# Optimization experiments

Measured on AMD Instinct MI355X. Metric: run time of the kernel, lower is better.

Reference implementation:

```python
import jax, jax.numpy as jnp
import numpy as np

N_NODES = 25000
N_EDGES = 400000
F_IN = 6
H = 128
NUM_CLASSES = 21
NUM_GAUSS = 16
Z_DIM = 2 * H + NUM_GAUSS  # 272


def setup_inputs() -> dict:
    key = jax.random.key(0)
    ks = jax.random.split(key, 16)
    inp = {
        "x": jax.random.normal(ks[0], (N_NODES, F_IN), dtype=jnp.float32),
        "edge_attr": jax.random.uniform(ks[1], (N_EDGES,), dtype=jnp.float32) * 8.0,
        "node_w": jax.random.normal(ks[2], (F_IN, H), dtype=jnp.float32) * 0.1,
        "node_b": jnp.zeros((H,), jnp.float32),
        "f1_w": jax.random.normal(ks[3], (Z_DIM, H), dtype=jnp.float32) * 0.05,
        "f1_b": jnp.zeros((H,), jnp.float32),
        "s1_w": jax.random.normal(ks[4], (Z_DIM, H), dtype=jnp.float32) * 0.05,
        "s1_b": jnp.zeros((H,), jnp.float32),
        "bn1_g": jnp.ones((H,), jnp.float32),
        "bn1_b": jnp.zeros((H,), jnp.float32),
        "f2_w": jax.random.normal(ks[5], (Z_DIM, H), dtype=jnp.float32) * 0.05,
        "f2_b": jnp.zeros((H,), jnp.float32),
        "s2_w": jax.random.normal(ks[6], (Z_DIM, H), dtype=jnp.float32) * 0.05,
        "s2_b": jnp.zeros((H,), jnp.float32),
        "bn2_g": jnp.ones((H,), jnp.float32),
        "bn2_b": jnp.zeros((H,), jnp.float32),
        "fc_w": jax.random.normal(ks[7], (H, NUM_CLASSES), dtype=jnp.float32) * 0.05,
        "fc_b": jnp.zeros((NUM_CLASSES,), jnp.float32),
        "edge_index": jax.random.randint(ks[8], (2, N_EDGES), 0, N_NODES, dtype=jnp.int64),
    }
    return inp


def gaussian_smearing(dist):
    # start=0, stop=8, num_gaussians=16
    offset = jnp.linspace(0.0, 8.0, NUM_GAUSS)
    coeff = -0.5 / (8.0 / (NUM_GAUSS - 1)) ** 2
    d = dist[:, None] - offset[None, :]  # [E, 16]
    return jnp.exp(coeff * d * d)


def cgconv(x, src, dst, e, fw, fb, sw, sb, gamma, beta):
    # PyG CGConv: z = cat([x_i, x_j, e]); msg = sigmoid(lin_f(z)) * softplus(lin_s(z))
    # aggr='add' into target i, then BatchNorm1d, then residual +x
    z = jnp.concatenate([x[dst], x[src], e], axis=-1)  # [E, 2H+16]
    msg = jax.nn.sigmoid(z @ fw + fb) * jax.nn.softplus(z @ sw + sb)  # [E, H]
    agg = jax.ops.segment_sum(msg, dst, num_segments=x.shape[0])  # [N, H]
    mu = jnp.mean(agg, axis=0)
    var = jnp.var(agg, axis=0)
    agg = (agg - mu) * jax.lax.rsqrt(var + 1e-5) * gamma + beta
    return agg + x


def reference(x, edge_attr, node_w, node_b, f1_w, f1_b, s1_w, s1_b, bn1_g, bn1_b,
              f2_w, f2_b, s2_w, s2_b, bn2_g, bn2_b, fc_w, fc_b, edge_index):
    src, dst = edge_index[0], edge_index[1]
    e = gaussian_smearing(edge_attr)  # [E, 16]
    h = x @ node_w + node_b  # [N, H]
    h = cgconv(h, src, dst, e, f1_w, f1_b, s1_w, s1_b, bn1_g, bn1_b)
    h = jax.nn.relu(h)
    # dropout p=0.1 is identity in eval mode
    h = cgconv(h, src, dst, e, f2_w, f2_b, s2_w, s2_b, bn2_g, bn2_b)
    h = jax.nn.relu(h)
    return h @ fc_w + fc_b  # [N, 21]
```

## Files before the change

kernel.cpp:

```cpp
#include <hip/hip_runtime.h>
#include <hip/hip_bf16.h>
#include <math.h>

#define NN 25000
#define NE 400000
#define HH 128
#define NH (NN*HH)
#define NBINS 2048

#define GS_STEP  (8.0f/15.0f)
#define GS_COEFF (-1.7578125f)
#define LOG2E    1.442695041f
#define LN2      0.6931471806f
#define BINSC    ((float)NBINS / 8.0f)

typedef float f32x2 __attribute__((ext_vector_type(2)));
typedef float f32x4 __attribute__((ext_vector_type(4)));
typedef short bf16x8 __attribute__((ext_vector_type(8)));

__device__ __forceinline__ f32x2 bf2_unpack(unsigned int u) {
  union { unsigned int i; float f; } lo, hi;
  lo.i = u << 16;
  hi.i = u & 0xffff0000u;
  f32x2 r; r.x = lo.f; r.y = hi.f;
  return r;
}

__device__ __forceinline__ unsigned short bf16_of(float f) {
  return __hip_bfloat16_raw(__float2bfloat16(f)).x;
}

__global__ __launch_bounds__(256) void k_prep(
    const float* __restrict__ f1w, const float* __restrict__ s1w,
    const float* __restrict__ f1b, const float* __restrict__ s1b,
    const float* __restrict__ f2w, const float* __restrict__ s2w,
    const float* __restrict__ f2b, const float* __restrict__ s2b,
    unsigned short* __restrict__ Wf1, float* __restrict__ bv1,
    unsigned short* __restrict__ L1,
    unsigned short* __restrict__ Wf2, float* __restrict__ bv2,
    unsigned short* __restrict__ L2, float* __restrict__ statsall,
    int* __restrict__ deg) {
  const int layer = blockIdx.y;
  const float* fw = layer ? f2w : f1w;
  const float* sw = layer ? s2w : s1w;
  const float* fb = layer ? f2b : f1b;
  const float* sb = layer ? s2b : s1b;
  unsigned short* Wf = layer ? Wf2 : Wf1;
  float* biasv = layer ? bv2 : bv1;
  unsigned short* LUT = layer ? L2 : L1;
  const int bx = blockIdx.x;
  const int tid = threadIdx.x;
  if (bx < 256) {
    if (bx == 0) statsall[layer * 256 + tid] = 0.f;
    if (layer == 0 && bx < 98) {
      const int i = bx * 256 + tid;
      if (i < NN) deg[i] = 0;
    }
    const int t = bx * 256 + tid;
    if (t < 512) biasv[t] = (t < 256) ? ((t & 1) ? sb[t >> 1] : fb[t >> 1]) : 0.f;
    const int j = t & 7;
    const int lane = (t >> 3) & 63;
    const int kt = (t >> 9) & 3;
    const int nt = t >> 11;
    const int k = 32 * kt + 8 * (lane >> 4) + j;
    const int c = 16 * nt + (lane & 15);
    const int cc = c & 255;
    const int row = ((c >= 256) ? 128 : 0) + k;
    const float* m = (cc & 1) ? sw : fw;
    Wf[t] = bf16_of(m[row * HH + (cc >> 1)]);
  } else {
    const int bin = (bx - 256) * 2 + (tid >> 7);
    if (bin > NBINS) return;
    const int j = tid & 127;
    const float* fw3 = fw + 256 * HH;
    const float* sw3 = sw + 256 * HH;
    const float d = (float)bin * (8.0f / (float)NBINS);
    f32x2 acc = 0.f;
#pragma unroll
    for (int k = 0; k < 16; ++k) {
      float tt = d - (float)k * GS_STEP;
      float ee = __expf(GS_COEFF * tt * tt);
      f32x2 w;
      w.x = fw3[k * HH + j];
      w.y = sw3[k * HH + j];
      acc = __builtin_elementwise_fma((f32x2)(ee), w, acc);
    }
    *(unsigned int*)&LUT[bin * 256 + 2 * j] =
        (unsigned int)bf16_of(acc.x) | ((unsigned int)bf16_of(acc.y) << 16);
  }
}

__device__ __forceinline__ void gemm_core(
    const unsigned short* As, const unsigned short* __restrict__ Wfrag,
    const float* __restrict__ biasv, int n0, int bn0,
    unsigned short* __restrict__ PDh, unsigned short* __restrict__ PSh,
    int tid) {
  const int w = tid >> 6;
  const int lane = tid & 63;
  const int mt0 = 2 * w;
  f32x4 acc[2][8];
#pragma unroll
  for (int mi = 0; mi < 2; ++mi)
#pragma unroll
    for (int nt = 0; nt < 8; ++nt) acc[mi][nt] = (f32x4)0.f;
  const int ntg0 = bn0 >> 4;
#pragma unroll
  for (int kt = 0; kt < 4; ++kt) {
    const bf16x8 a0 = *(const bf16x8*)&As[((mt0 * 4 + kt) * 64 + lane) * 8];
    const bf16x8 a1 = *(const bf16x8*)&As[(((mt0 + 1) * 4 + kt) * 64 + lane) * 8];
#pragma unroll
    for (int nt = 0; nt < 8; ++nt) {
      const bf16x8 b =
          *(const bf16x8*)&Wfrag[(((ntg0 + nt) * 4 + kt) * 64 + lane) * 8];
      acc[0][nt] = __builtin_amdgcn_mfma_f32_16x16x32_bf16(a0, b, acc[0][nt], 0, 0, 0);
      acc[1][nt] = __builtin_amdgcn_mfma_f32_16x16x32_bf16(a1, b, acc[1][nt], 0, 0, 0);
    }
  }
  const int colloc = lane & 15;
  const int rbase = (lane >> 4) * 4;
  const bool isPD = (bn0 < 256);
#pragma unroll
  for (int mi = 0; mi < 2; ++mi) {
#pragma unroll
    for (int nt = 0; nt < 8; ++nt) {
      const int c = bn0 + nt * 16 + colloc;
      const float bias = biasv[c];
#pragma unroll
      for (int r = 0; r < 4; ++r) {
        const int n = n0 + (mt0 + mi) * 16 + rbase + r;
        if (n < NN) {
          const float vv = acc[mi][nt][r] + bias;
          if (isPD) PDh[n * 256 + c] = bf16_of(vv);
          else PSh[n * 256 + (c - 256)] = bf16_of(vv);
        }
      }
    }
  }
}

__global__ __launch_bounds__(256) void k_gemm1(
    const float* __restrict__ x, const float* __restrict__ nw,
    const float* __restrict__ nb, const unsigned short* __restrict__ Wfrag,
    const float* __restrict__ biasv, float* __restrict__ h0,
    unsigned short* __restrict__ PDh, unsigned short* __restrict__ PSh,
    float* __restrict__ zb) {
  __shared__ unsigned short As[128 * 128];
  __shared__ float wn[6 * 128 + 128];
  const int tid = threadIdx.x;
  const int n0 = blockIdx.x * 128;
  const int bn0 = blockIdx.y * 128;
  const bool wr_h0 = (blockIdx.y == 0);
  for (int i = tid; i < 6 * 128 + 128; i += 256)
    wn[i] = (i < 6 * 128) ? nw[i] : nb[i - 6 * 128];
  if (blockIdx.y == 1) {
    const float4 z = {0.f, 0.f, 0.f, 0.f};
    for (int i = tid; i < 128 * 32; i += 256) {
      const int n = n0 + (i >> 5);
      if (n < NN) *(float4*)&zb[n * HH + (i & 31) * 4] = z;
    }
  }
  __syncthreads();
  {
    const int tn = tid >> 2;
    const int cj = tid & 3;
#pragma unroll
    for (int ii = 0; ii < 2; ++ii) {
      const int n = tn + 64 * ii;
      const int gn = n0 + n;
      float xr[6];
      if (gn < NN) {
#pragma unroll
        for (int q = 0; q < 6; ++q) xr[q] = x[gn * 6 + q];
      }
#pragma unroll
      for (int i = 0; i < 4; ++i) {
        const int c = cj + 4 * i;
        bf16x8 bv = (bf16x8)0;
        if (gn < NN) {
          float4 r0, r1;
#pragma unroll
          for (int j = 0; j < 8; ++j) {
            const int k = c * 8 + j;
            float acc = wn[6 * 128 + k];
#pragma unroll
            for (int q = 0; q < 6; ++q) acc = fmaf(xr[q], wn[q * 128 + k], acc);
            if (j < 4) (&r0.x)[j] = acc; else (&r1.x)[j - 4] = acc;
            bv[j] = (short)bf16_of(acc);
          }
          if (wr_h0) {
            *(float4*)&h0[gn * HH + c * 8] = r0;
            *(float4*)&h0[gn * HH + c * 8 + 4] = r1;
          }
        }
        const int slot = ((n >> 4) * 4 + (c >> 2)) * 64 + (n & 15) + 16 * (c & 3);
        *(bf16x8*)&As[slot * 8] = bv;
      }
    }
  }
  __syncthreads();
  gemm_core(As, Wfrag, biasv, n0, bn0, PDh, PSh, tid);
}

__global__ __launch_bounds__(256) void k_gemm_mfma(
    const float* __restrict__ h, const unsigned short* __restrict__ Wfrag,
    const float* __restrict__ biasv,
    unsigned short* __restrict__ PDh, unsigned short* __restrict__ PSh) {
  __shared__ unsigned short As[128 * 128];
  const int tid = threadIdx.x;
  const int n0 = blockIdx.x * 128;
  const int bn0 = blockIdx.y * 128;
  {
    const int tn = tid >> 2;
    const int cj = tid & 3;
#pragma unroll
    for (int ii = 0; ii < 2; ++ii) {
      const int n = tn + 64 * ii;
      const int gn = n0 + n;
#pragma unroll
      for (int i = 0; i < 4; ++i) {
        const int c = cj + 4 * i;
        bf16x8 bv;
        if (gn < NN) {
          const float4 p0 = *(const float4*)&h[gn * HH + c * 8];
          const float4 p1 = *(const float4*)&h[gn * HH + c * 8 + 4];
          bv[0] = (short)bf16_of(p0.x); bv[1] = (short)bf16_of(p0.y);
          bv[2] = (short)bf16_of(p0.z); bv[3] = (short)bf16_of(p0.w);
          bv[4] = (short)bf16_of(p1.x); bv[5] = (short)bf16_of(p1.y);
          bv[6] = (short)bf16_of(p1.z); bv[7] = (short)bf16_of(p1.w);
        } else {
          bv = (bf16x8)0;
        }
        const int slot = ((n >> 4) * 4 + (c >> 2)) * 64 + (n & 15) + 16 * (c & 3);
        *(bf16x8*)&As[slot * 8] = bv;
      }
    }
  }
  __syncthreads();
  gemm_core(As, Wfrag, biasv, n0, bn0, PDh, PSh, tid);
}

__global__ __launch_bounds__(256) void k_hist(
    const int* __restrict__ ei, int* __restrict__ deg, int* __restrict__ rank) {
  int e = blockIdx.x * 256 + threadIdx.x;
  if (e < NE) rank[e] = atomicAdd(&deg[ei[NE + e]], 1);
}

__global__ __launch_bounds__(1024) void k_scan(
    const int* __restrict__ deg, int* __restrict__ rowptr) {
  __shared__ int part[1024];
  const int tid = threadIdx.x;
  const int CH = (NN + 1023) / 1024;
  const int base = tid * CH;
  int s = 0;
  for (int i = 0; i < CH; ++i) {
    int n = base + i;
    if (n < NN) s += deg[n];
  }
  part[tid] = s;
  __syncthreads();
  for (int off = 1; off < 1024; off <<= 1) {
    int t = (tid >= off) ? part[tid - off] : 0;
    __syncthreads();
    part[tid] += t;
    __syncthreads();
  }
  int run = part[tid] - s;
  for (int i = 0; i < CH; ++i) {
    int n = base + i;
    if (n < NN) {
      rowptr[n] = run;
      run += deg[n];
    }
  }
}

__global__ __launch_bounds__(256) void k_scatter(
    const int* __restrict__ ei, const float* __restrict__ eattr,
    const int* __restrict__ rowptr, const int* __restrict__ rank,
    int2* __restrict__ emeta) {
  int e = blockIdx.x * 256 + threadIdx.x;
  if (e >= NE) return;
  const int dst = ei[NE + e];
  const int src = ei[e];
  const int bin = (int)(eattr[e] * BINSC + 0.5f);
  const int pos = rowptr[dst] + rank[e];
  emeta[pos] = make_int2(src | (dst << 16), bin << 8);
}

__global__ __launch_bounds__(256) void k_edge_sorted(
    const int2* __restrict__ emeta, const unsigned short* __restrict__ LUTh,
    const unsigned short* __restrict__ PDh, const unsigned short* __restrict__ PSh,
    float* __restrict__ agg) {
  const int tid = threadIdx.x;
  const int lane = tid & 63;
  const int w = __builtin_amdgcn_readfirstlane(tid >> 6);
  const int bid = blockIdx.x;
  const int xcd = bid & 7;
  const int idx = bid >> 3;
  const int sb = ((xcd < 5) ? xcd * 391 : 5 * 391 + (xcd - 5) * 390) + idx;
  const int e0 = sb * 128 + w * 32;
  const int u4 = 4 * lane;
  float m0 = 0.f, m1 = 0.f;
  int cur = -1;
  f32x2 a0 = 0.f, a1 = 0.f;
  uint2 b[4], v[4];
#pragma unroll
  for (int p = 0; p < 4; ++p) {
    const int2 md = emeta[e0 + p];
    b[p] = *(const uint2*)&PSh[((md.x & 0xffff) << 8) + u4];
    v[p] = *(const uint2*)&LUTh[md.y + u4];
  }
#pragma unroll
  for (int it = 0; it < 32; ++it) {
    const int sl = it & 3;
    const int dst = (int)((unsigned)emeta[e0 + it].x >> 16);
    if (dst != cur) {
      const uint2 ad = *(const uint2*)&PDh[(dst << 8) + u4];
      a0 = bf2_unpack(ad.x);
      a1 = bf2_unpack(ad.y);
      cur = dst;
    }
    const f32x2 bb0 = bf2_unpack(b[sl].x);
    const f32x2 bb1 = bf2_unpack(b[sl].y);
    const f32x2 w0 = bf2_unpack(v[sl].x);
    const f32x2 w1 = bf2_unpack(v[sl].y);
    if (it < 28) {
      const int2 mn = emeta[e0 + it + 4];
      b[sl] = *(const uint2*)&PSh[((mn.x & 0xffff) << 8) + u4];
      v[sl] = *(const uint2*)&LUTh[mn.y + u4];
    }
    const f32x2 fs0 = (a0 + bb0) + w0;
    const f32x2 fs1 = (a1 + bb1) + w1;
    const float ef0 = __builtin_amdgcn_exp2f(-fs0.x * LOG2E);
    const float ef1 = __builtin_amdgcn_exp2f(-fs1.x * LOG2E);
    const float et0 = __builtin_amdgcn_exp2f(-fabsf(fs0.y) * LOG2E);
    const float et1 = __builtin_amdgcn_exp2f(-fabsf(fs1.y) * LOG2E);
    const float sig0 = __builtin_amdgcn_rcpf(1.f + ef0);
    const float sig1 = __builtin_amdgcn_rcpf(1.f + ef1);
    const float sp0 = fmaxf(fs0.y, 0.f) + LN2 * __builtin_amdgcn_logf(1.f + et0);
    const float sp1 = fmaxf(fs1.y, 0.f) + LN2 * __builtin_amdgcn_logf(1.f + et1);
    m0 = fmaf(sig0, sp0, m0);
    m1 = fmaf(sig1, sp1, m1);
    bool fl = true;
    if (it < 31) fl = ((int)((unsigned)emeta[e0 + it + 1].x >> 16) != dst);
    if (fl) {
      atomicAdd(&agg[dst * HH + 2 * lane], m0);
      atomicAdd(&agg[dst * HH + 2 * lane + 1], m1);
      m0 = 0.f;
      m1 = 0.f;
    }
  }
}

__global__ __launch_bounds__(256) void k_stats(
    const float* __restrict__ agg, float* __restrict__ stats) {
  const int c = threadIdx.x & 127;
  const int slice = (blockIdx.x * 256 + threadIdx.x) >> 7;
  const int nslices = (gridDim.x * 256) >> 7;
  float s = 0.f, s2 = 0.f;
  for (int n = slice; n < NN; n += nslices) {
    float v = agg[n * HH + c];
    s += v;
    s2 = fmaf(v, v, s2);
  }
  atomicAdd(&stats[c], s);
  atomicAdd(&stats[HH + c], s2);
}

__global__ __launch_bounds__(256) void k_bn(
    const float* __restrict__ agg, float* __restrict__ hold,
    const float* __restrict__ stats, const float* __restrict__ g,
    const float* __restrict__ b, float* __restrict__ hnew) {
  int t = blockIdx.x * 256 + threadIdx.x;
  if (t >= NH) return;
  const int c = t & 127;
  const float inv_n = 1.f / (float)NN;
  const float mu = stats[c] * inv_n;
  const float var = stats[HH + c] * inv_n - mu * mu;
  const float rs = rsqrtf(var + 1e-5f);
  const float v = (agg[t] - mu) * rs * g[c] + b[c] + hold[t];
  hnew[t] = fmaxf(v, 0.f);
  hold[t] = 0.f;
}

__global__ __launch_bounds__(256) void k_fc(
    const float* __restrict__ agg, const float* __restrict__ hold,
    const float* __restrict__ stats, const float* __restrict__ g,
    const float* __restrict__ bb, const float* __restrict__ w,
    const float* __restrict__ b, float* __restrict__ out) {
  __shared__ float hs[8][128];
  __shared__ float scale[128], shift[128];
  const int tid = threadIdx.x;
  const int n0 = blockIdx.x * 8;
  if (tid < 128) {
    const float inv_n = 1.f / (float)NN;
    const float mu = stats[tid] * inv_n;
    const float var = stats[128 + tid] * inv_n - mu * mu;
    const float sc = rsqrtf(var + 1e-5f) * g[tid];
    scale[tid] = sc;
    shift[tid] = bb[tid] - mu * sc;
  }
  __syncthreads();
  {
    const int nl = tid >> 5;
    const int k0 = (tid & 31) * 4;
    const int gn = n0 + nl;
    if (gn < NN) {
      const float4 av = *(const float4*)&agg[gn * HH + k0];
      const float4 ov = *(const float4*)&hold[gn * HH + k0];
#pragma unroll
      for (int jj = 0; jj < 4; ++jj) {
        const int k = k0 + jj;
        const float a = (&av.x)[jj], o = (&ov.x)[jj];
        hs[nl][k] = fmaxf(fmaf(a, scale[k], shift[k]) + o, 0.f);
      }
    }
  }
  __syncthreads();
  const int ln = tid >> 5;
  const int m = tid & 31;
  const int n = n0 + ln;
  if (n >= NN || m >= 21) return;
  float acc = b[m];
#pragma unroll 4
  for (int k = 0; k < HH; ++k) acc = fmaf(hs[ln][k], w[k * 21 + m], acc);
  out[n * 21 + m] = acc;
}

extern "C" void kernel_launch(void* const* d_in, const int* in_sizes, int n_in,
                              void* d_out, int out_size, void* d_ws, size_t ws_size,
                              hipStream_t stream) {
  const float* x      = (const float*)d_in[0];
  const float* eattr  = (const float*)d_in[1];
  const float* node_w = (const float*)d_in[2];
  const float* node_b = (const float*)d_in[3];
  const float* f1w    = (const float*)d_in[4];
  const float* f1b    = (const float*)d_in[5];
  const float* s1w    = (const float*)d_in[6];
  const float* s1b    = (const float*)d_in[7];
  const float* bn1g   = (const float*)d_in[8];
  const float* bn1b   = (const float*)d_in[9];
  const float* f2w    = (const float*)d_in[10];
  const float* f2b    = (const float*)d_in[11];
  const float* s2w    = (const float*)d_in[12];
  const float* s2b    = (const float*)d_in[13];
  const float* bn2g   = (const float*)d_in[14];
  const float* bn2b   = (const float*)d_in[15];
  const float* fcw    = (const float*)d_in[16];
  const float* fcb    = (const float*)d_in[17];
  const int*   ei     = (const int*)d_in[18];
  float* out = (float*)d_out;

  float* ws   = (float*)d_ws;
  float* bufA = ws;
  float* bufB = ws + NH;
  unsigned short* PDh = (unsigned short*)(ws + 2 * (size_t)NH);
  unsigned short* PSh = (unsigned short*)(ws + 3 * (size_t)NH);
  float* stats1 = ws + 4 * (size_t)NH;
  float* stats2 = stats1 + 256;
  int*   deg    = (int*)(stats2 + 256);
  int*   rowptr = deg + NN;
  int*   rank   = rowptr + NN;
  int2*  emeta  = (int2*)(rank + NE);
  unsigned short* Wf1 = (unsigned short*)(emeta + NE);
  float* bv1    = (float*)(Wf1 + 65536);
  unsigned short* Wf2 = (unsigned short*)(bv1 + 512);
  float* bv2    = (float*)(Wf2 + 65536);
  unsigned short* lut1 = (unsigned short*)(bv2 + 512);
  unsigned short* lut2 = lut1 + (size_t)(NBINS + 1) * 256;

  const int g_edge  = NE / 128;
  const int g_bn    = (NH + 255) / 256;
  const int g_e256  = (NE + 255) / 256;
  const dim3 g_gemm((NN + 127) / 128, 4);
  const dim3 g_prep(256 + (NBINS + 2 + 1) / 2, 2);

  k_prep<<<g_prep, 256, 0, stream>>>(f1w, s1w, f1b, s1b, f2w, s2w, f2b, s2b,
                                     Wf1, bv1, lut1, Wf2, bv2, lut2,
                                     stats1, deg);

  k_hist<<<g_e256, 256, 0, stream>>>(ei, deg, rank);
  k_scan<<<1, 1024, 0, stream>>>(deg, rowptr);
  k_scatter<<<g_e256, 256, 0, stream>>>(ei, eattr, rowptr, rank, emeta);

  k_gemm1<<<g_gemm, 256, 0, stream>>>(x, node_w, node_b, Wf1, bv1, bufA,
                                      PDh, PSh, bufB);
  k_edge_sorted<<<g_edge, 256, 0, stream>>>(emeta, lut1, PDh, PSh, bufB);
  k_stats<<<256, 256, 0, stream>>>(bufB, stats1);
  k_bn<<<g_bn, 256, 0, stream>>>(bufB, bufA, stats1, bn1g, bn1b, bufB);

  k_gemm_mfma<<<g_gemm, 256, 0, stream>>>(bufB, Wf2, bv2, PDh, PSh);
  k_edge_sorted<<<g_edge, 256, 0, stream>>>(emeta, lut2, PDh, PSh, bufA);
  k_stats<<<256, 256, 0, stream>>>(bufA, stats2);

  k_fc<<<(NN + 7) / 8, 256, 0, stream>>>(bufA, bufB, stats2, bn2g, bn2b,
                                         fcw, fcb, out);
}
```

Before: 303.2 us.

## Fuse histogram into prep kernel, prefetch dst rows, vectorize stats

Three changes. The degree-histogram kernel is folded into the prep launch as a third grid slice, and deg is cleared with a memset. The edge kernel now prefetches the next distinct destination's PDh row a few edges ahead, so the gather latency at segment boundaries is hidden. The BN stats kernel reads float4 per thread on half as many blocks. Fusing the histogram saves one launch, but it adds a memset, and the prep grid now includes idle blocks.

```diff
diff --git a/kernel.cpp b/kernel.cpp
--- a/kernel.cpp
+++ b/kernel.cpp
@@ -39,7 +39,16 @@
     unsigned short* __restrict__ L1,
     unsigned short* __restrict__ Wf2, float* __restrict__ bv2,
     unsigned short* __restrict__ L2, float* __restrict__ statsall,
-    int* __restrict__ deg) {
+    int* __restrict__ deg, const int* __restrict__ ei,
+    int* __restrict__ rank) {
+  const int bx = blockIdx.x;
+  const int tid = threadIdx.x;
+  if (blockIdx.y == 2) {
+    int e = bx * 256 + tid;
+    if (e < NE) rank[e] = atomicAdd(&deg[ei[NE + e]], 1);
+    return;
+  }
+  if (bx >= 1281) return;
   const int layer = blockIdx.y;
   const float* fw = layer ? f2w : f1w;
   const float* sw = layer ? s2w : s1w;
@@ -48,14 +57,8 @@
   unsigned short* Wf = layer ? Wf2 : Wf1;
   float* biasv = layer ? bv2 : bv1;
   unsigned short* LUT = layer ? L2 : L1;
-  const int bx = blockIdx.x;
-  const int tid = threadIdx.x;
   if (bx < 256) {
     if (bx == 0) statsall[layer * 256 + tid] = 0.f;
-    if (layer == 0 && bx < 98) {
-      const int i = bx * 256 + tid;
-      if (i < NN) deg[i] = 0;
-    }
     const int t = bx * 256 + tid;
     if (t < 512) biasv[t] = (t < 256) ? ((t & 1) ? sb[t >> 1] : fb[t >> 1]) : 0.f;
     const int j = t & 7;
@@ -239,12 +242,6 @@
   gemm_core(As, Wfrag, biasv, n0, bn0, PDh, PSh, tid);
 }
 
-__global__ __launch_bounds__(256) void k_hist(
-    const int* __restrict__ ei, int* __restrict__ deg, int* __restrict__ rank) {
-  int e = blockIdx.x * 256 + threadIdx.x;
-  if (e < NE) rank[e] = atomicAdd(&deg[ei[NE + e]], 1);
-}
-
 __global__ __launch_bounds__(1024) void k_scan(
     const int* __restrict__ deg, int* __restrict__ rowptr) {
   __shared__ int part[1024];
@@ -304,6 +301,8 @@
   int cur = -1;
   f32x2 a0 = 0.f, a1 = 0.f;
   uint2 b[4], v[4];
+  int pend_dst = (int)((unsigned)emeta[e0].x >> 16);
+  uint2 pend = *(const uint2*)&PDh[(pend_dst << 8) + u4];
 #pragma unroll
   for (int p = 0; p < 4; ++p) {
     const int2 md = emeta[e0 + p];
@@ -315,7 +314,9 @@
     const int sl = it & 3;
     const int dst = (int)((unsigned)emeta[e0 + it].x >> 16);
     if (dst != cur) {
-      const uint2 ad = *(const uint2*)&PDh[(dst << 8) + u4];
+      uint2 ad;
+      if (dst == pend_dst) ad = pend;
+      else ad = *(const uint2*)&PDh[(dst << 8) + u4];
       a0 = bf2_unpack(ad.x);
       a1 = bf2_unpack(ad.y);
       cur = dst;
@@ -328,6 +329,12 @@
       const int2 mn = emeta[e0 + it + 4];
       b[sl] = *(const uint2*)&PSh[((mn.x & 0xffff) << 8) + u4];
       v[sl] = *(const uint2*)&LUTh[mn.y + u4];
+      const int d4 = (int)((unsigned)mn.x >> 16);
+      const int d3 = (int)((unsigned)emeta[e0 + it + 3].x >> 16);
+      if (d4 != d3) {
+        pend = *(const uint2*)&PDh[(d4 << 8) + u4];
+        pend_dst = d4;
+      }
     }
     const f32x2 fs0 = (a0 + bb0) + w0;
     const f32x2 fs1 = (a1 + bb1) + w1;
@@ -354,17 +361,23 @@
 
 __global__ __launch_bounds__(256) void k_stats(
     const float* __restrict__ agg, float* __restrict__ stats) {
-  const int c = threadIdx.x & 127;
-  const int slice = (blockIdx.x * 256 + threadIdx.x) >> 7;
-  const int nslices = (gridDim.x * 256) >> 7;
-  float s = 0.f, s2 = 0.f;
+  const int c4 = (threadIdx.x & 31) * 4;
+  const int slice = blockIdx.x * 8 + (threadIdx.x >> 5);
+  const int nslices = gridDim.x * 8;
+  f32x4 s = (f32x4)0.f, s2 = (f32x4)0.f;
   for (int n = slice; n < NN; n += nslices) {
-    float v = agg[n * HH + c];
-    s += v;
-    s2 = fmaf(v, v, s2);
-  }
-  atomicAdd(&stats[c], s);
-  atomicAdd(&stats[HH + c], s2);
+    const float4 vv = *(const float4*)&agg[n * HH + c4];
+    s.x += vv.x; s.y += vv.y; s.z += vv.z; s.w += vv.w;
+    s2.x = fmaf(vv.x, vv.x, s2.x);
+    s2.y = fmaf(vv.y, vv.y, s2.y);
+    s2.z = fmaf(vv.z, vv.z, s2.z);
+    s2.w = fmaf(vv.w, vv.w, s2.w);
+  }
+#pragma unroll
+  for (int j = 0; j < 4; ++j) {
+    atomicAdd(&stats[c4 + j], s[j]);
+    atomicAdd(&stats[HH + c4 + j], s2[j]);
+  }
 }
 
 __global__ __launch_bounds__(256) void k_bn(
@@ -473,25 +486,26 @@
   const int g_bn    = (NH + 255) / 256;
   const int g_e256  = (NE + 255) / 256;
   const dim3 g_gemm((NN + 127) / 128, 4);
-  const dim3 g_prep(256 + (NBINS + 2 + 1) / 2, 2);
+  const dim3 g_prep(1563, 3);
+
+  hipMemsetAsync(deg, 0, NN * 4, stream);
 
   k_prep<<<g_prep, 256, 0, stream>>>(f1w, s1w, f1b, s1b, f2w, s2w, f2b, s2b,
                                      Wf1, bv1, lut1, Wf2, bv2, lut2,
-                                     stats1, deg);
-
-  k_hist<<<g_e256, 256, 0, stream>>>(ei, deg, rank);
+                                     stats1, deg, ei, rank);
+
   k_scan<<<1, 1024, 0, stream>>>(deg, rowptr);
   k_scatter<<<g_e256, 256, 0, stream>>>(ei, eattr, rowptr, rank, emeta);
 
   k_gemm1<<<g_gemm, 256, 0, stream>>>(x, node_w, node_b, Wf1, bv1, bufA,
                                       PDh, PSh, bufB);
   k_edge_sorted<<<g_edge, 256, 0, stream>>>(emeta, lut1, PDh, PSh, bufB);
-  k_stats<<<256, 256, 0, stream>>>(bufB, stats1);
+  k_stats<<<128, 256, 0, stream>>>(bufB, stats1);
   k_bn<<<g_bn, 256, 0, stream>>>(bufB, bufA, stats1, bn1g, bn1b, bufB);
 
   k_gemm_mfma<<<g_gemm, 256, 0, stream>>>(bufB, Wf2, bv2, PDh, PSh);
   k_edge_sorted<<<g_edge, 256, 0, stream>>>(emeta, lut2, PDh, PSh, bufA);
-  k_stats<<<256, 256, 0, stream>>>(bufA, stats2);
+  k_stats<<<128, 256, 0, stream>>>(bufA, stats2);
 
   k_fc<<<(NN + 7) / 8, 256, 0, stream>>>(bufA, bufB, stats2, bn2g, bn2b,
                                          fcw, fcb, out);
```

Result: slower. 470.4 us (+55.1%).
